# Performance work log

Hardware: AMD Instinct MI355X
Metric: run time of the kernel (lower is better)

## Reference

```python
import jax, jax.numpy as jnp
import numpy as np

N_NODES = 5000
N_EDGES = 40000
NUM_ATOM_TYPES = 100
HID = 32            # multiplicity of 0e and 1o in irreps_hidden
EDGE_ATTR_DIM = 8
NUM_BOND_TYPES = 5
OUT_SCALARS = 2 * 6 + 1  # max_charge=6 -> 13x0e
CUTOFF = 5.0
SQRT3 = 1.7320508075688772


def _sh(edge_vec):
    # o3.SphericalHarmonics('1x0e + 1x1o', normalize=True, normalization='component')
    d = jnp.sqrt(jnp.sum(edge_vec * edge_vec, axis=-1) + 1e-12)
    n = edge_vec / d[:, None]
    sh0 = jnp.ones(edge_vec.shape[0], edge_vec.dtype)          # [E]
    sh1 = SQRT3 * n[:, (1, 2, 0)]                              # [E,3], e3nn (y,z,x) order
    return sh0, sh1, d


def _soft_one_hot(d):
    # e3nn.math.soft_one_hot_linspace(d, 0, cutoff, 8, basis='gaussian', cutoff=True)
    values = jnp.linspace(0.0, CUTOFF, EDGE_ATTR_DIM + 2)[1:-1]
    step = CUTOFF / (EDGE_ATTR_DIM + 1)
    diff = (d[:, None] - values[None, :]) / step
    return jnp.exp(-diff * diff) / 1.12


def _mlp(x, W0, b0, W1, b1):
    # ScalarMLP(in, out, hidden=[in], SiLU)
    return jax.nn.silu(x @ W0 + b0) @ W1 + b1


def _tp_init(s, sh0, sh1, w):
    # FCTP(32x0e, 1x0e+1x1o -> 32x0e+32x1o); paths: 0e*0e->0e, 0e*1o->1o
    E = s.shape[0]
    w1 = w[:, : HID * HID].reshape(E, HID, HID)
    w2 = w[:, HID * HID :].reshape(E, HID, HID)
    c = 1.0 / np.sqrt(HID)  # fan-in = 32 per output irrep
    out_s = c * jnp.einsum('eu,euw->ew', s * sh0[:, None], w1)
    out_v = c * jnp.einsum('eu,ei,euw->ewi', s, sh1, w2)
    return out_s, out_v


def _tp_hidden(s, v, sh0, sh1, w):
    # FCTP(32x0e+32x1o, 1x0e+1x1o -> 32x0e+32x1o)
    # path order: 0e*0e->0e, 0e*1o->1o, 1o*0e->1o, 1o*1o->0e
    E = s.shape[0]
    ws = w.reshape(E, 4, HID, HID)
    c = 1.0 / np.sqrt(2 * HID)  # fan-in = 64 per output irrep
    dot = jnp.einsum('eui,ei->eu', v, sh1) / SQRT3  # CG(1,1->0) = delta/sqrt(3)
    out_s = c * (jnp.einsum('eu,euw->ew', s * sh0[:, None], ws[:, 0]) +
                 jnp.einsum('eu,euw->ew', dot, ws[:, 3]))
    out_v = c * (jnp.einsum('eu,ei,euw->ewi', s, sh1, ws[:, 1]) +
                 jnp.einsum('eui,euw->ewi', v * sh0[:, None, None], ws[:, 2]))
    return out_s, out_v


def _edge_tp(s1, v1, s2, v2, sh0, sh1, w):
    # FCTP(64x0e+64x1o (concat of two hidden), 1x0e+1x1o -> 5x0e)
    # blocks in concat order: s_src, v_src, s_dst, v_dst
    E = s1.shape[0]
    ws = w.reshape(E, 4, HID, NUM_BOND_TYPES)
    c = 1.0 / np.sqrt(4 * HID)  # fan-in = 128
    d1 = jnp.einsum('eui,ei->eu', v1, sh1) / SQRT3
    d2 = jnp.einsum('eui,ei->eu', v2, sh1) / SQRT3
    return c * (jnp.einsum('eu,euw->ew', s1 * sh0[:, None], ws[:, 0]) +
                jnp.einsum('eu,euw->ew', d1, ws[:, 1]) +
                jnp.einsum('eu,euw->ew', s2 * sh0[:, None], ws[:, 2]) +
                jnp.einsum('eu,euw->ew', d2, ws[:, 3]))


def _scatter_mean(ms, mv, dst, n):
    cnt = jax.ops.segment_sum(jnp.ones(dst.shape[0], ms.dtype), dst, num_segments=n)
    cnt = jnp.maximum(cnt, 1.0)
    s = jax.ops.segment_sum(ms, dst, num_segments=n) / cnt[:, None]
    v = jax.ops.segment_sum(mv, dst, num_segments=n) / cnt[:, None, None]
    return s, v


def setup_inputs() -> dict:
    key = jax.random.key(0)
    ks = jax.random.split(key, 16)
    def w(k, shape, fan_in):
        return jax.random.normal(k, shape, dtype=jnp.float32) / np.sqrt(fan_in)
    inp = {}
    inp['coordinates'] = jax.random.normal(ks[0], (N_NODES, 3), dtype=jnp.float32) * 1.5
    inp['atom_types'] = jax.random.randint(ks[1], (N_NODES,), 0, NUM_ATOM_TYPES)
    inp['edge_index'] = jax.random.randint(ks[2], (2, N_EDGES), 0, N_NODES)
    inp['atom_embed'] = jax.random.normal(ks[3], (NUM_ATOM_TYPES, HID), dtype=jnp.float32)
    inp['ip_W0'] = w(ks[4], (EDGE_ATTR_DIM, EDGE_ATTR_DIM), EDGE_ATTR_DIM)
    inp['ip_b0'] = jnp.zeros((EDGE_ATTR_DIM,), jnp.float32)
    inp['ip_W1'] = w(ks[5], (EDGE_ATTR_DIM, 2 * HID * HID), EDGE_ATTR_DIM)
    inp['ip_b1'] = jnp.zeros((2 * HID * HID,), jnp.float32)
    inp['ly_W0'] = w(ks[6], (EDGE_ATTR_DIM, EDGE_ATTR_DIM), EDGE_ATTR_DIM)
    inp['ly_b0'] = jnp.zeros((EDGE_ATTR_DIM,), jnp.float32)
    inp['ly_W1'] = w(ks[7], (EDGE_ATTR_DIM, 4 * HID * HID), EDGE_ATTR_DIM)
    inp['ly_b1'] = jnp.zeros((4 * HID * HID,), jnp.float32)
    inp['ly_Ws'] = jax.random.normal(ks[8], (HID, HID), dtype=jnp.float32)
    inp['ly_Wv'] = jax.random.normal(ks[9], (HID, HID), dtype=jnp.float32)
    inp['et_W0'] = w(ks[10], (EDGE_ATTR_DIM, EDGE_ATTR_DIM), EDGE_ATTR_DIM)
    inp['et_b0'] = jnp.zeros((EDGE_ATTR_DIM,), jnp.float32)
    inp['et_W1'] = w(ks[11], (EDGE_ATTR_DIM, 4 * HID * NUM_BOND_TYPES), EDGE_ATTR_DIM)
    inp['et_b1'] = jnp.zeros((4 * HID * NUM_BOND_TYPES,), jnp.float32)
    inp['no_W1'] = jax.random.normal(ks[12], (HID, OUT_SCALARS), dtype=jnp.float32)
    inp['no_W2'] = jax.random.normal(ks[13], (OUT_SCALARS, OUT_SCALARS), dtype=jnp.float32)
    return inp


def reference(coordinates, atom_types, edge_index, atom_embed,
              ip_W0, ip_b0, ip_W1, ip_b1,
              ly_W0, ly_b0, ly_W1, ly_b1, ly_Ws, ly_Wv,
              et_W0, et_b0, et_W1, et_b1, no_W1, no_W2):
    n = coordinates.shape[0]
    src, dst = edge_index[0], edge_index[1]
    edge_vec = coordinates[dst] - coordinates[src]
    sh0, sh1, d = _sh(edge_vec)
    edge_attr = _soft_one_hot(d)                              # [E,8]
    # initial projector: Conv(32x0e -> 32x0e+32x1o)
    s0 = atom_embed[atom_types]                               # [N,32]
    w_ip = _mlp(edge_attr, ip_W0, ip_b0, ip_W1, ip_b1)        # [E,2048]
    ms, mv = _tp_init(s0[src], sh0, sh1, w_ip)
    s, v = _scatter_mean(ms, mv, dst, n)                      # [N,32],[N,32,3]
    # one LinearSelfInteraction(Conv) layer
    w_ly = _mlp(edge_attr, ly_W0, ly_b0, ly_W1, ly_b1)        # [E,4096]
    ms, mv = _tp_hidden(s[src], v[src], sh0, sh1, w_ly)
    cs, cv = _scatter_mean(ms, mv, dst, n)
    lc = 1.0 / np.sqrt(HID)  # e3nn o3.Linear normalization
    s = cs + lc * (s @ ly_Ws)
    v = cv + lc * jnp.einsum('eui,uw->ewi', v, ly_Wv)
    # edge output: FCTP([h_src, h_dst], edge_sh) with radial weights
    w_et = _mlp(edge_attr, et_W0, et_b0, et_W1, et_b1)        # [E,640]
    edge_out = _edge_tp(s[src], v[src], s[dst], v[dst], sh0, sh1, w_et)  # [E,5]
    # node output MLP on detached scalar channel (13x0e)
    sd = jax.lax.stop_gradient(s)
    h = jax.nn.silu(sd @ no_W1 / np.sqrt(HID))
    node_out = h @ no_W2 / np.sqrt(OUT_SCALARS)               # [N,13]
    return edge_out, node_out
```

## Files before the change

### kernel.cpp

```cpp
#include <hip/hip_runtime.h>

#define NN 5000
#define NE 40000

typedef unsigned int u32;
typedef unsigned short u16;
typedef __fp16 h16x2 __attribute__((ext_vector_type(2)));
typedef _Float16 f16x8 __attribute__((ext_vector_type(8)));
typedef __attribute__((ext_vector_type(4))) float f32x4;

union AF { u32 u[4]; f16x8 v; uint4 q; };

__device__ __forceinline__ float siluf(float x) { return x / (1.f + __expf(-x)); }

__device__ __forceinline__ u32 f2bf_u(float f) {
  u32 x = __float_as_uint(f);
  return (x + 0x7FFFu + ((x >> 16) & 1u)) >> 16;
}
__device__ __forceinline__ u16 f2bf(float f) { return (u16)f2bf_u(f); }
__device__ __forceinline__ u32 packbf2(float lo, float hi) {
  return f2bf_u(lo) | (f2bf_u(hi) << 16);
}
__device__ __forceinline__ u32 pkh2(float a, float b) {
  union { h16x2 h; u32 u; } r;
  r.h = __builtin_amdgcn_cvt_pkrtz(a, b);
  return r.u;
}
__device__ __forceinline__ u16 f2h(float v) {
  _Float16 h = (_Float16)v;
  return *(u16*)&h;
}
__device__ __forceinline__ void unpack8(uint4 q, float* f) {
  f[0] = __uint_as_float(q.x << 16); f[1] = __uint_as_float(q.x & 0xFFFF0000u);
  f[2] = __uint_as_float(q.y << 16); f[3] = __uint_as_float(q.y & 0xFFFF0000u);
  f[4] = __uint_as_float(q.z << 16); f[5] = __uint_as_float(q.z & 0xFFFF0000u);
  f[6] = __uint_as_float(q.w << 16); f[7] = __uint_as_float(q.w & 0xFFFF0000u);
}
__device__ __forceinline__ float dot8f(const float* h, const float* w, float init) {
  float a = init;
#pragma unroll
  for (int k = 0; k < 8; k++) a = fmaf(h[k], w[k], a);
  return a;
}
__device__ __forceinline__ void mlp8(const float* ea, const float* __restrict__ W0,
                                     const float* __restrict__ b0, float* h) {
#pragma unroll
  for (int j = 0; j < 8; j++) {
    float a = b0[j];
#pragma unroll
    for (int i = 0; i < 8; i++) a += ea[i] * W0[i*8 + j];
    h[j] = siluf(a);
  }
}
__device__ __forceinline__ AF mkfrag(float hs, const float* s) {
  AF a;
  a.u[0] = pkh2(hs*s[0], hs*s[1]);
  a.u[1] = pkh2(hs*s[2], hs*s[3]);
  a.u[2] = pkh2(hs*s[4], hs*s[5]);
  a.u[3] = pkh2(hs*s[6], hs*s[7]);
  return a;
}

__global__ __launch_bounds__(256) void k_prep(
    const float* __restrict__ ipW1, const float* __restrict__ ipb1,
    u16* __restrict__ ipT) {
  int t0 = blockIdx.x*2304 + threadIdx.x*9;
#pragma unroll
  for (int j = 0; j < 9; j++) {
    int t = t0 + j;
    int kch = t >> 9, rem = t & 511;
    int col = rem >> 3, kk = rem & 7;
    int k = kch*8 + kk;
    int pth = col >> 5, w = col & 31;
    float v = (k < 256) ? ipW1[(k >> 5)*2048 + pth*1024 + (k & 31)*32 + w]
                        : ipb1[pth*1024 + (k - 256)*32 + w];
    ipT[t] = f2h(v);
  }
}

__global__ __launch_bounds__(256) void k_conv1(
    const float* __restrict__ coords, const int* __restrict__ eidx,
    const float* __restrict__ emb, const int* __restrict__ atype,
    const float* __restrict__ ipW0, const float* __restrict__ ipb0,
    const float* __restrict__ lyW0, const float* __restrict__ lyb0,
    const float* __restrict__ etW0, const float* __restrict__ etb0,
    const float* __restrict__ lyW1, const float* __restrict__ lyb1,
    const u16* __restrict__ ipT,
    float* __restrict__ sh, float* __restrict__ h_ly, float* __restrict__ h_et,
    int* __restrict__ cur, int* __restrict__ perm,
    u16* __restrict__ msg, u16* __restrict__ lyT) {
  if (blockIdx.x >= 625) {
    int b = blockIdx.x - 625;
    int h = b >> 3;
    int t0 = (b & 7)*2304 + threadIdx.x*9;
#pragma unroll
    for (int j = 0; j < 9; j++) {
      int t = t0 + j;
      int kch = t >> 9, rem = t & 511;
      int col = rem >> 3, kk = rem & 7;
      int k = kch*8 + kk;
      int basec = (h == 0) ? ((col >> 5)*1024 + (col & 31))
                           : ((col < 32) ? (2048 + col) : (3072 + (col - 32)));
      float v = (k < 256) ? lyW1[(k >> 5)*4096 + basec + (k & 31)*32]
                          : lyb1[basec + (k - 256)*32];
      lyT[h*18432 + t] = f2h(v);
    }
    return;
  }
  int wid = threadIdx.x >> 6, lane = threadIdx.x & 63;
  int tile = blockIdx.x*4 + wid;
  int m = lane & 15, q = lane >> 4;
  int e = tile*16 + m;
  int s = eidx[e], d = eidx[NE + e];
  int t = 0;
  if (q == 0) {
    int* cp = &cur[d];
    atomicCAS(cp, (int)0xAAAAAAAA, 0);
    t = atomicAdd(cp, 1);
    if (t < 64) perm[d*64 + t] = e;
  }
  int srow = atype[s];
  float vx = coords[d*3+0] - coords[s*3+0];
  float vy = coords[d*3+1] - coords[s*3+1];
  float vz = coords[d*3+2] - coords[s*3+2];
  float dist = sqrtf(vx*vx + vy*vy + vz*vz + 1e-12f);
  float dinv = 1.f / dist;
  const float SQ3 = 1.7320508075688772f;
  float sh0 = SQ3 * vy * dinv;
  float sh1 = SQ3 * vz * dinv;
  float sh2 = SQ3 * vx * dinv;
  float ea[8];
  const float step = 5.f / 9.f;
#pragma unroll
  for (int jj = 0; jj < 8; jj++) {
    float diff = (dist - step * (float)(jj+1)) * (9.f / 5.f);
    ea[jj] = __expf(-diff*diff) * (1.f / 1.12f);
  }
  float hip[8], hly[8], het[8];
  mlp8(ea, ipW0, ipb0, hip);
  mlp8(ea, lyW0, lyb0, hly);
  mlp8(ea, etW0, etb0, het);
  if (q == 0) {
    sh[e*3+0] = sh0; sh[e*3+1] = sh1; sh[e*3+2] = sh2;
    { float4 f0 = {hly[0],hly[1],hly[2],hly[3]}, f1 = {hly[4],hly[5],hly[6],hly[7]};
      *(float4*)&h_ly[e*8] = f0; *(float4*)&h_ly[e*8+4] = f1; }
    { float4 f0 = {het[0],het[1],het[2],het[3]}, f1 = {het[4],het[5],het[6],het[7]};
      *(float4*)&h_et[e*8] = f0; *(float4*)&h_et[e*8+4] = f1; }
  }
  float4 sA = *(const float4*)&emb[srow*32 + q*8];
  float4 sB = *(const float4*)&emb[srow*32 + q*8 + 4];
  float sf[8] = {sA.x,sA.y,sA.z,sA.w,sB.x,sB.y,sB.z,sB.w};
  f32x4 acc0 = {0.f,0.f,0.f,0.f}, acc1 = acc0, acc2 = acc0, acc3 = acc0;
  const float cs = 0.17677669529663687f;
#pragma unroll
  for (int ks = 0; ks < 9; ks++) {
    float hs = (ks < 8) ? hip[ks] : 1.f;
    AF a = mkfrag(hs, sf);
    int c2 = (ks*4 + q)*64;
    AF b0, b1f, b2, b3;
    b0.q  = *(const uint4*)&ipT[(c2 +  0 + m)*8];
    b1f.q = *(const uint4*)&ipT[(c2 + 16 + m)*8];
    b2.q  = *(const uint4*)&ipT[(c2 + 32 + m)*8];
    b3.q  = *(const uint4*)&ipT[(c2 + 48 + m)*8];
    acc0 = __builtin_amdgcn_mfma_f32_16x16x32_f16(a.v, b0.v,  acc0, 0, 0, 0);
    acc1 = __builtin_amdgcn_mfma_f32_16x16x32_f16(a.v, b1f.v, acc1, 0, 0, 0);
    acc2 = __builtin_amdgcn_mfma_f32_16x16x32_f16(a.v, b2.v,  acc2, 0, 0, 0);
    acc3 = __builtin_amdgcn_mfma_f32_16x16x32_f16(a.v, b3.v,  acc3, 0, 0, 0);
  }
#pragma unroll
  for (int r = 0; r < 4; r++) {
    int et = tile*16 + q*4 + r;
    u16* mp = msg + (size_t)et*128;
    mp[m]      = f2bf(cs*acc0[r]);
    mp[16 + m] = f2bf(cs*acc1[r]);
    float s0v = __shfl(sh0, q*4 + r, 64);
    float s1v = __shfl(sh1, q*4 + r, 64);
    float s2v = __shfl(sh2, q*4 + r, 64);
    float m0 = cs*acc2[r], m1 = cs*acc3[r];
    mp[32 +      m] = f2bf(m0*s0v);
    mp[64 +      m] = f2bf(m0*s1v);
    mp[96 +      m] = f2bf(m0*s2v);
    mp[32 + 16 + m] = f2bf(m1*s0v);
    mp[64 + 16 + m] = f2bf(m1*s1v);
    mp[96 + 16 + m] = f2bf(m1*s2v);
  }
}

__global__ __launch_bounds__(256) void k_conv2(
    const float* __restrict__ hE, const float* __restrict__ sh,
    const float* __restrict__ s1, const float* __restrict__ v1soa,
    const int* __restrict__ eidx, const u16* __restrict__ lyT,
    u16* __restrict__ msgA, u16* __restrict__ msgB) {
  int wid = threadIdx.x >> 6, lane = threadIdx.x & 63;
  const bool scalarHalf = blockIdx.x < 625;
  int blk = scalarHalf ? blockIdx.x : blockIdx.x - 625;
  int tile = blk*4 + wid;
  int m = lane & 15, q = lane >> 4;
  const u16* Bg = lyT + (scalarHalf ? 0 : 18432);
  const float c = 0.125f;
  int e = tile*16 + m;
  int srcn = eidx[e];
  float4 hA = *(const float4*)&hE[e*8];
  float4 hB = *(const float4*)&hE[e*8 + 4];
  float hf[8] = {hA.x,hA.y,hA.z,hA.w,hB.x,hB.y,hB.z,hB.w};

  if (scalarHalf) {
    float4 sA = *(const float4*)&s1[srcn*32 + q*8];
    float4 sB = *(const float4*)&s1[srcn*32 + q*8 + 4];
    float sf[8] = {sA.x,sA.y,sA.z,sA.w,sB.x,sB.y,sB.z,sB.w};
    f32x4 acc0 = {0.f,0.f,0.f,0.f}, acc1 = acc0, acc2 = acc0, acc3 = acc0;
#pragma unroll
    for (int ks = 0; ks < 9; ks++) {
      float hs = (ks < 8) ? hf[ks] : 1.f;
      AF a = mkfrag(hs, sf);
      int c2 = (ks*4 + q)*64;
      AF b0, b1f, b2, b3;
      b0.q  = *(const uint4*)&Bg[(c2 +  0 + m)*8];
      b1f.q = *(const uint4*)&Bg[(c2 + 16 + m)*8];
      b2.q  = *(const uint4*)&Bg[(c2 + 32 + m)*8];
      b3.q  = *(const uint4*)&Bg[(c2 + 48 + m)*8];
      acc0 = __builtin_amdgcn_mfma_f32_16x16x32_f16(a.v, b0.v,  acc0, 0, 0, 0);
      acc1 = __builtin_amdgcn_mfma_f32_16x16x32_f16(a.v, b1f.v, acc1, 0, 0, 0);
      acc2 = __builtin_amdgcn_mfma_f32_16x16x32_f16(a.v, b2.v,  acc2, 0, 0, 0);
      acc3 = __builtin_amdgcn_mfma_f32_16x16x32_f16(a.v, b3.v,  acc3, 0, 0, 0);
    }
#pragma unroll
    for (int r = 0; r < 4; r++) {
      int et = tile*16 + q*4 + r;
      u16* mp = msgA + (size_t)et*128;
      mp[m]      = f2bf(c*acc0[r]);
      mp[16 + m] = f2bf(c*acc1[r]);
      float s0v = sh[et*3+0], s1v = sh[et*3+1], s2v = sh[et*3+2];
      float m0 = c*acc2[r], m1 = c*acc3[r];
      mp[32 +      m] = f2bf(m0*s0v);
      mp[64 +      m] = f2bf(m0*s1v);
      mp[96 +      m] = f2bf(m0*s2v);
      mp[32 + 16 + m] = f2bf(m1*s0v);
      mp[64 + 16 + m] = f2bf(m1*s1v);
      mp[96 + 16 + m] = f2bf(m1*s2v);
    }
  } else {
    const float is3 = 0.5773502691896258f;
    float vf[3][8];
#pragma unroll
    for (int i = 0; i < 3; i++) {
      float4 aa = *(const float4*)&v1soa[i*160000 + srcn*32 + q*8];
      float4 bb = *(const float4*)&v1soa[i*160000 + srcn*32 + q*8 + 4];
      vf[i][0]=aa.x; vf[i][1]=aa.y; vf[i][2]=aa.z; vf[i][3]=aa.w;
      vf[i][4]=bb.x; vf[i][5]=bb.y; vf[i][6]=bb.z; vf[i][7]=bb.w;
    }
    float es0 = sh[e*3+0], es1 = sh[e*3+1], es2 = sh[e*3+2];
    float df[8];
#pragma unroll
    for (int j = 0; j < 8; j++)
      df[j] = (vf[0][j]*es0 + vf[1][j]*es1 + vf[2][j]*es2) * is3;
    f32x4 z = {0.f,0.f,0.f,0.f};
    f32x4 aV00 = z, aV01 = z, aV10 = z, aV11 = z, aV20 = z, aV21 = z, aD0 = z, aD1 = z;
#pragma unroll
    for (int ks = 0; ks < 9; ks++) {
      float hs = (ks < 8) ? hf[ks] : 1.f;
      int c2 = (ks*4 + q)*64;
      AF b0, b1f, b2, b3;
      b0.q  = *(const uint4*)&Bg[(c2 +  0 + m)*8];
      b1f.q = *(const uint4*)&Bg[(c2 + 16 + m)*8];
      b2.q  = *(const uint4*)&Bg[(c2 + 32 + m)*8];
      b3.q  = *(const uint4*)&Bg[(c2 + 48 + m)*8];
      AF a0 = mkfrag(hs, vf[0]);
      AF a1 = mkfrag(hs, vf[1]);
      AF a2 = mkfrag(hs, vf[2]);
      AF ad = mkfrag(hs, df);
      aV00 = __builtin_amdgcn_mfma_f32_16x16x32_f16(a0.v, b0.v,  aV00, 0, 0, 0);
      aV01 = __builtin_amdgcn_mfma_f32_16x16x32_f16(a0.v, b1f.v, aV01, 0, 0, 0);
      aV10 = __builtin_amdgcn_mfma_f32_16x16x32_f16(a1.v, b0.v,  aV10, 0, 0, 0);
      aV11 = __builtin_amdgcn_mfma_f32_16x16x32_f16(a1.v, b1f.v, aV11, 0, 0, 0);
      aV20 = __builtin_amdgcn_mfma_f32_16x16x32_f16(a2.v, b0.v,  aV20, 0, 0, 0);
      aV21 = __builtin_amdgcn_mfma_f32_16x16x32_f16(a2.v, b1f.v, aV21, 0, 0, 0);
      aD0  = __builtin_amdgcn_mfma_f32_16x16x32_f16(ad.v, b2.v,  aD0,  0, 0, 0);
      aD1  = __builtin_amdgcn_mfma_f32_16x16x32_f16(ad.v, b3.v,  aD1,  0, 0, 0);
    }
#pragma unroll
    for (int r = 0; r < 4; r++) {
      int et = tile*16 + q*4 + r;
      u16* mp = msgB + (size_t)et*128;
      mp[m]      = f2bf(c*aD0[r]);
      mp[16 + m] = f2bf(c*aD1[r]);
      mp[32 +      m] = f2bf(c*aV00[r]);
      mp[32 + 16 + m] = f2bf(c*aV01[r]);
      mp[64 +      m] = f2bf(c*aV10[r]);
      mp[64 + 16 + m] = f2bf(c*aV11[r]);
      mp[96 +      m] = f2bf(c*aV20[r]);
      mp[96 + 16 + m] = f2bf(c*aV21[r]);
    }
  }
}

__global__ __launch_bounds__(256) void k_gather1(
    const u16* __restrict__ msg, const int* __restrict__ perm,
    const int* __restrict__ cur, float* __restrict__ s1,
    float* __restrict__ v1soa) {
  __shared__ int pe[2][64];
  int ln = threadIdx.x >> 7, c = threadIdx.x & 127;
  int n = blockIdx.x*2 + ln;
  int deg = min(cur[n], 64);
  if (c < 64) pe[ln][c] = perm[n*64 + c];
  __syncthreads();
  float acc = 0.f;
  int j = 0;
  for (; j + 4 <= deg; j += 4) {
    int e0 = pe[ln][j], e1 = pe[ln][j+1], e2 = pe[ln][j+2], e3 = pe[ln][j+3];
    float x0 = __uint_as_float(((u32)msg[(size_t)e0*128 + c]) << 16);
    float x1 = __uint_as_float(((u32)msg[(size_t)e1*128 + c]) << 16);
    float x2 = __uint_as_float(((u32)msg[(size_t)e2*128 + c]) << 16);
    float x3 = __uint_as_float(((u32)msg[(size_t)e3*128 + c]) << 16);
    acc += (x0 + x1) + (x2 + x3);
  }
  for (; j < deg; j++)
    acc += __uint_as_float(((u32)msg[(size_t)pe[ln][j]*128 + c]) << 16);
  acc /= (float)max(deg, 1);
  if (c < 32) s1[n*32 + c] = acc;
  else { int i = (c-32) >> 5, w = (c-32) & 31; v1soa[i*160000 + n*32 + w] = acc; }
}

__global__ __launch_bounds__(256) void k_gather2(
    const u16* __restrict__ msgA, const u16* __restrict__ msgB,
    const int* __restrict__ perm, const int* __restrict__ cur,
    const float* __restrict__ s1, const float* __restrict__ v1soa,
    const float* __restrict__ Ws, const float* __restrict__ Wv,
    const float* __restrict__ noW1, const float* __restrict__ noW2,
    float* __restrict__ s2, float* __restrict__ v2, float* __restrict__ outN) {
  __shared__ int pe[2][64];
  __shared__ float sb[2][32];
  __shared__ float hb[2][13];
  int ln = threadIdx.x >> 7, c = threadIdx.x & 127;
  int n = blockIdx.x*2 + ln;
  int deg = min(cur[n], 64);
  if (c < 64) pe[ln][c] = perm[n*64 + c];
  __syncthreads();
  float acc = 0.f;
  int j = 0;
  for (; j + 4 <= deg; j += 4) {
    int e0 = pe[ln][j], e1 = pe[ln][j+1], e2 = pe[ln][j+2], e3 = pe[ln][j+3];
    float x0 = __uint_as_float(((u32)msgA[(size_t)e0*128 + c]) << 16)
             + __uint_as_float(((u32)msgB[(size_t)e0*128 + c]) << 16);
    float x1 = __uint_as_float(((u32)msgA[(size_t)e1*128 + c]) << 16)
             + __uint_as_float(((u32)msgB[(size_t)e1*128 + c]) << 16);
    float x2 = __uint_as_float(((u32)msgA[(size_t)e2*128 + c]) << 16)
             + __uint_as_float(((u32)msgB[(size_t)e2*128 + c]) << 16);
    float x3 = __uint_as_float(((u32)msgA[(size_t)e3*128 + c]) << 16)
             + __uint_as_float(((u32)msgB[(size_t)e3*128 + c]) << 16);
    acc += (x0 + x1) + (x2 + x3);
  }
  for (; j < deg; j++) {
    int e = pe[ln][j];
    acc += __uint_as_float(((u32)msgA[(size_t)e*128 + c]) << 16)
         + __uint_as_float(((u32)msgB[(size_t)e*128 + c]) << 16);
  }
  acc /= (float)max(deg, 1);
  const float lc = 0.17677669529663687f;
  if (c < 32) {
    float ss = 0.f;
#pragma unroll 8
    for (int u = 0; u < 32; u++) ss += s1[n*32 + u] * Ws[u*32 + c];
    float val = acc + lc*ss;
    s2[n*32 + c] = val;
    sb[ln][c] = val;
  } else {
    int i = (c-32) >> 5, w = (c-32) & 31;
    float sv = 0.f;
#pragma unroll 8
    for (int u = 0; u < 32; u++) sv += v1soa[i*160000 + n*32 + u] * Wv[u*32 + w];
    v2[n*96 + w*3 + i] = acc + lc*sv;
  }
  __syncthreads();
  const float i32 = 0.17677669529663687f;
  if (c < 13) {
    float a = 0.f;
#pragma unroll 8
    for (int u = 0; u < 32; u++) a += sb[ln][u] * noW1[u*13 + c];
    hb[ln][c] = siluf(a * i32);
  }
  __syncthreads();
  const float i13 = 0.2773500981126146f;
  if (c < 13) {
    float a = 0.f;
#pragma unroll
    for (int j2 = 0; j2 < 13; j2++) a += hb[ln][j2] * noW2[j2*13 + c];
    outN[n*13 + c] = a * i13;
  }
}

__global__ __launch_bounds__(256) void k_e3(
    const float* __restrict__ hE, const float* __restrict__ sh,
    const float* __restrict__ s2, const float* __restrict__ v2,
    const int* __restrict__ eidx,
    const float* __restrict__ W1, const float* __restrict__ b1,
    float* __restrict__ out) {
  __shared__ uint4 WQ[640];
  __shared__ float BQ[640];
  for (int t = threadIdx.x; t < 640; t += 256) {
    int u = t & 31, pw = t >> 5, p2 = pw / 5, w = pw - p2*5;
    int col = p2*160 + u*5 + w;
    const float* s = W1 + col;
    uint4 q;
    q.x = packbf2(s[0],      s[640]);
    q.y = packbf2(s[1280],   s[1920]);
    q.z = packbf2(s[2560],   s[3200]);
    q.w = packbf2(s[3840],   s[4480]);
    WQ[t] = q;
    BQ[t] = b1[col];
  }
  __syncthreads();
  const int g = threadIdx.x >> 5, tw = threadIdx.x & 31;
  const float c = 0.08838834764831845f;
  const float is3 = 0.5773502691896258f;
  for (int p = blockIdx.x*8 + g; p*2 < NE; p += gridDim.x*8) {
    int e0 = p*2, e1 = e0 + 1;
    float h0[8], h1[8];
    {
      float4 qa = *(const float4*)&hE[e0*8];
      float4 qb = *(const float4*)&hE[e0*8+4];
      h0[0]=qa.x; h0[1]=qa.y; h0[2]=qa.z; h0[3]=qa.w;
      h0[4]=qb.x; h0[5]=qb.y; h0[6]=qb.z; h0[7]=qb.w;
      float4 qc = *(const float4*)&hE[e1*8];
      float4 qd = *(const float4*)&hE[e1*8+4];
      h1[0]=qc.x; h1[1]=qc.y; h1[2]=qc.z; h1[3]=qc.w;
      h1[4]=qd.x; h1[5]=qd.y; h1[6]=qd.z; h1[7]=qd.w;
    }
    int sA = eidx[e0], dA = eidx[NE+e0];
    int sB = eidx[e1], dB = eidx[NE+e1];
    float sa0 = sh[e0*3+0], sa1 = sh[e0*3+1], sa2 = sh[e0*3+2];
    float sb0 = sh[e1*3+0], sb1 = sh[e1*3+1], sb2 = sh[e1*3+2];
    float c00 = s2[sA*32 + tw];
    float c01 = (v2[sA*96+tw*3+0]*sa0 + v2[sA*96+tw*3+1]*sa1 + v2[sA*96+tw*3+2]*sa2) * is3;
    float c02 = s2[dA*32 + tw];
    float c03 = (v2[dA*96+tw*3+0]*sa0 + v2[dA*96+tw*3+1]*sa1 + v2[dA*96+tw*3+2]*sa2) * is3;
    float c10 = s2[sB*32 + tw];
    float c11 = (v2[sB*96+tw*3+0]*sb0 + v2[sB*96+tw*3+1]*sb1 + v2[sB*96+tw*3+2]*sb2) * is3;
    float c12 = s2[dB*32 + tw];
    float c13 = (v2[dB*96+tw*3+0]*sb0 + v2[dB*96+tw*3+1]*sb1 + v2[dB*96+tw*3+2]*sb2) * is3;
    float part0[5] = {0,0,0,0,0};
    float part1[5] = {0,0,0,0,0};
#pragma unroll
    for (int pp = 0; pp < 4; pp++) {
      float cp0 = (pp==0) ? c00 : (pp==1) ? c01 : (pp==2) ? c02 : c03;
      float cp1 = (pp==0) ? c10 : (pp==1) ? c11 : (pp==2) ? c12 : c13;
#pragma unroll
      for (int w = 0; w < 5; w++) {
        int idx = (pp*5 + w)*32 + tw;
        float f[8];
        unpack8(WQ[idx], f);
        float bv = BQ[idx];
        part0[w] = fmaf(cp0, dot8f(h0, f, bv), part0[w]);
        part1[w] = fmaf(cp1, dot8f(h1, f, bv), part1[w]);
      }
    }
#pragma unroll
    for (int off = 16; off > 0; off >>= 1)
#pragma unroll
      for (int w = 0; w < 5; w++) {
        part0[w] += __shfl_xor(part0[w], off, 32);
        part1[w] += __shfl_xor(part1[w], off, 32);
      }
    float outv = 0.f;
#pragma unroll
    for (int w = 0; w < 5; w++) {
      if (tw == w)     outv = part0[w];
      if (tw == 5 + w) outv = part1[w];
    }
    if (tw < 10) out[e0*5 + tw] = c * outv;
  }
}

extern "C" void kernel_launch(void* const* d_in, const int* in_sizes, int n_in,
                              void* d_out, int out_size, void* d_ws, size_t ws_size,
                              hipStream_t stream) {
  (void)in_sizes; (void)n_in; (void)out_size; (void)ws_size;
  const float* coords = (const float*)d_in[0];
  const int*   atype  = (const int*)d_in[1];
  const int*   eidx   = (const int*)d_in[2];
  const float* emb    = (const float*)d_in[3];
  const float* ipW0 = (const float*)d_in[4];
  const float* ipb0 = (const float*)d_in[5];
  const float* ipW1 = (const float*)d_in[6];
  const float* ipb1 = (const float*)d_in[7];
  const float* lyW0 = (const float*)d_in[8];
  const float* lyb0 = (const float*)d_in[9];
  const float* lyW1 = (const float*)d_in[10];
  const float* lyb1 = (const float*)d_in[11];
  const float* lyWs = (const float*)d_in[12];
  const float* lyWv = (const float*)d_in[13];
  const float* etW0 = (const float*)d_in[14];
  const float* etb0 = (const float*)d_in[15];
  const float* etW1 = (const float*)d_in[16];
  const float* etb1 = (const float*)d_in[17];
  const float* noW1 = (const float*)d_in[18];
  const float* noW2 = (const float*)d_in[19];

  float* ws = (float*)d_ws;
  float* sh    = ws;
  float* h_ly  = ws + 440000;
  float* h_et  = ws + 760000;
  float* s1    = ws + 1240000;
  float* v1soa = ws + 1400000;
  float* s2    = ws + 1880000;
  float* v2    = ws + 2040000;
  int*   cur   = (int*)(ws + 2520000);
  int*   perm  = (int*)(ws + 2525000);
  u16*   msgA  = (u16*)(ws + 2845000);
  u16*   msgB  = (u16*)(ws + 5405000);
  u16*   lyT   = (u16*)(ws + 7965000);
  u16*   ipT   = (u16*)(ws + 7983432);

  float* outE = (float*)d_out;
  float* outN = (float*)d_out + NE*5;

  k_prep<<<8, 256, 0, stream>>>(ipW1, ipb1, ipT);
  k_conv1<<<641, 256, 0, stream>>>(coords, eidx, emb, atype,
                                   ipW0, ipb0, lyW0, lyb0, etW0, etb0,
                                   lyW1, lyb1, ipT,
                                   sh, h_ly, h_et, cur, perm, msgA, lyT);
  k_gather1<<<NN/2, 256, 0, stream>>>(msgA, perm, cur, s1, v1soa);
  k_conv2<<<1250, 256, 0, stream>>>(h_ly, sh, s1, v1soa, eidx, lyT, msgA, msgB);
  k_gather2<<<NN/2, 256, 0, stream>>>(msgA, msgB, perm, cur, s1, v1soa,
                                      lyWs, lyWv, noW1, noW2, s2, v2, outN);
  k_e3<<<1024, 256, 0, stream>>>(h_et, sh, s2, v2, eidx, etW1, etb1, outE);
}
```

Baseline: 164.5 us.

## Split conv1 and conv2 edge tiles across two wavefronts by output half

Each 16-edge tile in k_conv1 and k_conv2 is now handled by two wavefronts, each computing half of the MFMA output columns. This doubles the grid sizes to spread the work over more waves and cuts the per-wave accumulator register count, which should help occupancy and latency hiding. The cost is redundant per-edge setup in both waves, such as the edge geometry, radial basis, MLP and source feature loads. In the vector branch of k_conv2, one wave also needs all three vector components to form the dot product.

```diff
diff --git a/kernel.cpp b/kernel.cpp
--- a/kernel.cpp
+++ b/kernel.cpp
@@ -89,8 +89,8 @@
     float* __restrict__ sh, float* __restrict__ h_ly, float* __restrict__ h_et,
     int* __restrict__ cur, int* __restrict__ perm,
     u16* __restrict__ msg, u16* __restrict__ lyT) {
-  if (blockIdx.x >= 625) {
-    int b = blockIdx.x - 625;
+  if (blockIdx.x >= 1250) {
+    int b = blockIdx.x - 1250;
     int h = b >> 3;
     int t0 = (b & 7)*2304 + threadIdx.x*9;
 #pragma unroll
@@ -108,15 +108,15 @@
     return;
   }
   int wid = threadIdx.x >> 6, lane = threadIdx.x & 63;
-  int tile = blockIdx.x*4 + wid;
+  int gw = blockIdx.x*4 + wid;
+  int tile = gw >> 1, half = gw & 1;
   int m = lane & 15, q = lane >> 4;
   int e = tile*16 + m;
   int s = eidx[e], d = eidx[NE + e];
-  int t = 0;
-  if (q == 0) {
+  if (half == 0 && q == 0) {
     int* cp = &cur[d];
     atomicCAS(cp, (int)0xAAAAAAAA, 0);
-    t = atomicAdd(cp, 1);
+    int t = atomicAdd(cp, 1);
     if (t < 64) perm[d*64 + t] = e;
   }
   int srow = atype[s];
@@ -136,53 +136,72 @@
     float diff = (dist - step * (float)(jj+1)) * (9.f / 5.f);
     ea[jj] = __expf(-diff*diff) * (1.f / 1.12f);
   }
-  float hip[8], hly[8], het[8];
+  float hip[8];
   mlp8(ea, ipW0, ipb0, hip);
-  mlp8(ea, lyW0, lyb0, hly);
-  mlp8(ea, etW0, etb0, het);
-  if (q == 0) {
-    sh[e*3+0] = sh0; sh[e*3+1] = sh1; sh[e*3+2] = sh2;
-    { float4 f0 = {hly[0],hly[1],hly[2],hly[3]}, f1 = {hly[4],hly[5],hly[6],hly[7]};
-      *(float4*)&h_ly[e*8] = f0; *(float4*)&h_ly[e*8+4] = f1; }
-    { float4 f0 = {het[0],het[1],het[2],het[3]}, f1 = {het[4],het[5],het[6],het[7]};
-      *(float4*)&h_et[e*8] = f0; *(float4*)&h_et[e*8+4] = f1; }
+  if (half == 0) {
+    float hly[8], het[8];
+    mlp8(ea, lyW0, lyb0, hly);
+    mlp8(ea, etW0, etb0, het);
+    if (q == 0) {
+      sh[e*3+0] = sh0; sh[e*3+1] = sh1; sh[e*3+2] = sh2;
+      { float4 f0 = {hly[0],hly[1],hly[2],hly[3]}, f1 = {hly[4],hly[5],hly[6],hly[7]};
+        *(float4*)&h_ly[e*8] = f0; *(float4*)&h_ly[e*8+4] = f1; }
+      { float4 f0 = {het[0],het[1],het[2],het[3]}, f1 = {het[4],het[5],het[6],het[7]};
+        *(float4*)&h_et[e*8] = f0; *(float4*)&h_et[e*8+4] = f1; }
+    }
   }
   float4 sA = *(const float4*)&emb[srow*32 + q*8];
   float4 sB = *(const float4*)&emb[srow*32 + q*8 + 4];
   float sf[8] = {sA.x,sA.y,sA.z,sA.w,sB.x,sB.y,sB.z,sB.w};
-  f32x4 acc0 = {0.f,0.f,0.f,0.f}, acc1 = acc0, acc2 = acc0, acc3 = acc0;
   const float cs = 0.17677669529663687f;
-#pragma unroll
-  for (int ks = 0; ks < 9; ks++) {
-    float hs = (ks < 8) ? hip[ks] : 1.f;
-    AF a = mkfrag(hs, sf);
-    int c2 = (ks*4 + q)*64;
-    AF b0, b1f, b2, b3;
-    b0.q  = *(const uint4*)&ipT[(c2 +  0 + m)*8];
-    b1f.q = *(const uint4*)&ipT[(c2 + 16 + m)*8];
-    b2.q  = *(const uint4*)&ipT[(c2 + 32 + m)*8];
-    b3.q  = *(const uint4*)&ipT[(c2 + 48 + m)*8];
-    acc0 = __builtin_amdgcn_mfma_f32_16x16x32_f16(a.v, b0.v,  acc0, 0, 0, 0);
-    acc1 = __builtin_amdgcn_mfma_f32_16x16x32_f16(a.v, b1f.v, acc1, 0, 0, 0);
-    acc2 = __builtin_amdgcn_mfma_f32_16x16x32_f16(a.v, b2.v,  acc2, 0, 0, 0);
-    acc3 = __builtin_amdgcn_mfma_f32_16x16x32_f16(a.v, b3.v,  acc3, 0, 0, 0);
-  }
-#pragma unroll
-  for (int r = 0; r < 4; r++) {
-    int et = tile*16 + q*4 + r;
-    u16* mp = msg + (size_t)et*128;
-    mp[m]      = f2bf(cs*acc0[r]);
-    mp[16 + m] = f2bf(cs*acc1[r]);
-    float s0v = __shfl(sh0, q*4 + r, 64);
-    float s1v = __shfl(sh1, q*4 + r, 64);
-    float s2v = __shfl(sh2, q*4 + r, 64);
-    float m0 = cs*acc2[r], m1 = cs*acc3[r];
-    mp[32 +      m] = f2bf(m0*s0v);
-    mp[64 +      m] = f2bf(m0*s1v);
-    mp[96 +      m] = f2bf(m0*s2v);
-    mp[32 + 16 + m] = f2bf(m1*s0v);
-    mp[64 + 16 + m] = f2bf(m1*s1v);
-    mp[96 + 16 + m] = f2bf(m1*s2v);
+  if (half == 0) {
+    f32x4 acc0 = {0.f,0.f,0.f,0.f}, acc1 = acc0;
+#pragma unroll
+    for (int ks = 0; ks < 9; ks++) {
+      float hs = (ks < 8) ? hip[ks] : 1.f;
+      AF a = mkfrag(hs, sf);
+      int c2 = (ks*4 + q)*64;
+      AF b0, b1f;
+      b0.q  = *(const uint4*)&ipT[(c2 +  0 + m)*8];
+      b1f.q = *(const uint4*)&ipT[(c2 + 16 + m)*8];
+      acc0 = __builtin_amdgcn_mfma_f32_16x16x32_f16(a.v, b0.v,  acc0, 0, 0, 0);
+      acc1 = __builtin_amdgcn_mfma_f32_16x16x32_f16(a.v, b1f.v, acc1, 0, 0, 0);
+    }
+#pragma unroll
+    for (int r = 0; r < 4; r++) {
+      int et = tile*16 + q*4 + r;
+      u16* mp = msg + (size_t)et*128;
+      mp[m]      = f2bf(cs*acc0[r]);
+      mp[16 + m] = f2bf(cs*acc1[r]);
+    }
+  } else {
+    f32x4 acc2 = {0.f,0.f,0.f,0.f}, acc3 = acc2;
+#pragma unroll
+    for (int ks = 0; ks < 9; ks++) {
+      float hs = (ks < 8) ? hip[ks] : 1.f;
+      AF a = mkfrag(hs, sf);
+      int c2 = (ks*4 + q)*64;
+      AF b2, b3;
+      b2.q = *(const uint4*)&ipT[(c2 + 32 + m)*8];
+      b3.q = *(const uint4*)&ipT[(c2 + 48 + m)*8];
+      acc2 = __builtin_amdgcn_mfma_f32_16x16x32_f16(a.v, b2.v, acc2, 0, 0, 0);
+      acc3 = __builtin_amdgcn_mfma_f32_16x16x32_f16(a.v, b3.v, acc3, 0, 0, 0);
+    }
+#pragma unroll
+    for (int r = 0; r < 4; r++) {
+      int et = tile*16 + q*4 + r;
+      u16* mp = msg + (size_t)et*128;
+      float s0v = __shfl(sh0, q*4 + r, 64);
+      float s1v = __shfl(sh1, q*4 + r, 64);
+      float s2v = __shfl(sh2, q*4 + r, 64);
+      float m0 = cs*acc2[r], m1 = cs*acc3[r];
+      mp[32 +      m] = f2bf(m0*s0v);
+      mp[64 +      m] = f2bf(m0*s1v);
+      mp[96 +      m] = f2bf(m0*s2v);
+      mp[32 + 16 + m] = f2bf(m1*s0v);
+      mp[64 + 16 + m] = f2bf(m1*s1v);
+      mp[96 + 16 + m] = f2bf(m1*s2v);
+    }
   }
 }
 
@@ -192,11 +211,12 @@
     const int* __restrict__ eidx, const u16* __restrict__ lyT,
     u16* __restrict__ msgA, u16* __restrict__ msgB) {
   int wid = threadIdx.x >> 6, lane = threadIdx.x & 63;
-  const bool scalarHalf = blockIdx.x < 625;
-  int blk = scalarHalf ? blockIdx.x : blockIdx.x - 625;
-  int tile = blk*4 + wid;
+  int gw = blockIdx.x*4 + wid;
+  const bool scalarKind = gw < 5000;
+  int t2 = scalarKind ? gw : gw - 5000;
+  int tile = t2 >> 1, half = t2 & 1;
   int m = lane & 15, q = lane >> 4;
-  const u16* Bg = lyT + (scalarHalf ? 0 : 18432);
+  const u16* Bg = lyT + (scalarKind ? 0 : 18432);
   const float c = 0.125f;
   int e = tile*16 + m;
   int srcn = eidx[e];
@@ -204,92 +224,135 @@
   float4 hB = *(const float4*)&hE[e*8 + 4];
   float hf[8] = {hA.x,hA.y,hA.z,hA.w,hB.x,hB.y,hB.z,hB.w};
 
-  if (scalarHalf) {
+  if (scalarKind) {
     float4 sA = *(const float4*)&s1[srcn*32 + q*8];
     float4 sB = *(const float4*)&s1[srcn*32 + q*8 + 4];
     float sf[8] = {sA.x,sA.y,sA.z,sA.w,sB.x,sB.y,sB.z,sB.w};
-    f32x4 acc0 = {0.f,0.f,0.f,0.f}, acc1 = acc0, acc2 = acc0, acc3 = acc0;
-#pragma unroll
-    for (int ks = 0; ks < 9; ks++) {
-      float hs = (ks < 8) ? hf[ks] : 1.f;
-      AF a = mkfrag(hs, sf);
-      int c2 = (ks*4 + q)*64;
-      AF b0, b1f, b2, b3;
-      b0.q  = *(const uint4*)&Bg[(c2 +  0 + m)*8];
-      b1f.q = *(const uint4*)&Bg[(c2 + 16 + m)*8];
-      b2.q  = *(const uint4*)&Bg[(c2 + 32 + m)*8];
-      b3.q  = *(const uint4*)&Bg[(c2 + 48 + m)*8];
-      acc0 = __builtin_amdgcn_mfma_f32_16x16x32_f16(a.v, b0.v,  acc0, 0, 0, 0);
-      acc1 = __builtin_amdgcn_mfma_f32_16x16x32_f16(a.v, b1f.v, acc1, 0, 0, 0);
-      acc2 = __builtin_amdgcn_mfma_f32_16x16x32_f16(a.v, b2.v,  acc2, 0, 0, 0);
-      acc3 = __builtin_amdgcn_mfma_f32_16x16x32_f16(a.v, b3.v,  acc3, 0, 0, 0);
-    }
-#pragma unroll
-    for (int r = 0; r < 4; r++) {
-      int et = tile*16 + q*4 + r;
-      u16* mp = msgA + (size_t)et*128;
-      mp[m]      = f2bf(c*acc0[r]);
-      mp[16 + m] = f2bf(c*acc1[r]);
-      float s0v = sh[et*3+0], s1v = sh[et*3+1], s2v = sh[et*3+2];
-      float m0 = c*acc2[r], m1 = c*acc3[r];
-      mp[32 +      m] = f2bf(m0*s0v);
-      mp[64 +      m] = f2bf(m0*s1v);
-      mp[96 +      m] = f2bf(m0*s2v);
-      mp[32 + 16 + m] = f2bf(m1*s0v);
-      mp[64 + 16 + m] = f2bf(m1*s1v);
-      mp[96 + 16 + m] = f2bf(m1*s2v);
+    if (half == 0) {
+      f32x4 acc0 = {0.f,0.f,0.f,0.f}, acc1 = acc0;
+#pragma unroll
+      for (int ks = 0; ks < 9; ks++) {
+        float hs = (ks < 8) ? hf[ks] : 1.f;
+        AF a = mkfrag(hs, sf);
+        int c2 = (ks*4 + q)*64;
+        AF b0, b1f;
+        b0.q  = *(const uint4*)&Bg[(c2 +  0 + m)*8];
+        b1f.q = *(const uint4*)&Bg[(c2 + 16 + m)*8];
+        acc0 = __builtin_amdgcn_mfma_f32_16x16x32_f16(a.v, b0.v,  acc0, 0, 0, 0);
+        acc1 = __builtin_amdgcn_mfma_f32_16x16x32_f16(a.v, b1f.v, acc1, 0, 0, 0);
+      }
+#pragma unroll
+      for (int r = 0; r < 4; r++) {
+        int et = tile*16 + q*4 + r;
+        u16* mp = msgA + (size_t)et*128;
+        mp[m]      = f2bf(c*acc0[r]);
+        mp[16 + m] = f2bf(c*acc1[r]);
+      }
+    } else {
+      f32x4 acc2 = {0.f,0.f,0.f,0.f}, acc3 = acc2;
+#pragma unroll
+      for (int ks = 0; ks < 9; ks++) {
+        float hs = (ks < 8) ? hf[ks] : 1.f;
+        AF a = mkfrag(hs, sf);
+        int c2 = (ks*4 + q)*64;
+        AF b2, b3;
+        b2.q = *(const uint4*)&Bg[(c2 + 32 + m)*8];
+        b3.q = *(const uint4*)&Bg[(c2 + 48 + m)*8];
+        acc2 = __builtin_amdgcn_mfma_f32_16x16x32_f16(a.v, b2.v, acc2, 0, 0, 0);
+        acc3 = __builtin_amdgcn_mfma_f32_16x16x32_f16(a.v, b3.v, acc3, 0, 0, 0);
+      }
+#pragma unroll
+      for (int r = 0; r < 4; r++) {
+        int et = tile*16 + q*4 + r;
+        u16* mp = msgA + (size_t)et*128;
+        float s0v = sh[et*3+0], s1v = sh[et*3+1], s2v = sh[et*3+2];
+        float m0 = c*acc2[r], m1 = c*acc3[r];
+        mp[32 +      m] = f2bf(m0*s0v);
+        mp[64 +      m] = f2bf(m0*s1v);
+        mp[96 +      m] = f2bf(m0*s2v);
+        mp[32 + 16 + m] = f2bf(m1*s0v);
+        mp[64 + 16 + m] = f2bf(m1*s1v);
+        mp[96 + 16 + m] = f2bf(m1*s2v);
+      }
     }
   } else {
     const float is3 = 0.5773502691896258f;
-    float vf[3][8];
-#pragma unroll
-    for (int i = 0; i < 3; i++) {
-      float4 aa = *(const float4*)&v1soa[i*160000 + srcn*32 + q*8];
-      float4 bb = *(const float4*)&v1soa[i*160000 + srcn*32 + q*8 + 4];
-      vf[i][0]=aa.x; vf[i][1]=aa.y; vf[i][2]=aa.z; vf[i][3]=aa.w;
-      vf[i][4]=bb.x; vf[i][5]=bb.y; vf[i][6]=bb.z; vf[i][7]=bb.w;
-    }
-    float es0 = sh[e*3+0], es1 = sh[e*3+1], es2 = sh[e*3+2];
-    float df[8];
-#pragma unroll
-    for (int j = 0; j < 8; j++)
-      df[j] = (vf[0][j]*es0 + vf[1][j]*es1 + vf[2][j]*es2) * is3;
-    f32x4 z = {0.f,0.f,0.f,0.f};
-    f32x4 aV00 = z, aV01 = z, aV10 = z, aV11 = z, aV20 = z, aV21 = z, aD0 = z, aD1 = z;
-#pragma unroll
-    for (int ks = 0; ks < 9; ks++) {
-      float hs = (ks < 8) ? hf[ks] : 1.f;
-      int c2 = (ks*4 + q)*64;
-      AF b0, b1f, b2, b3;
-      b0.q  = *(const uint4*)&Bg[(c2 +  0 + m)*8];
-      b1f.q = *(const uint4*)&Bg[(c2 + 16 + m)*8];
-      b2.q  = *(const uint4*)&Bg[(c2 + 32 + m)*8];
-      b3.q  = *(const uint4*)&Bg[(c2 + 48 + m)*8];
-      AF a0 = mkfrag(hs, vf[0]);
-      AF a1 = mkfrag(hs, vf[1]);
-      AF a2 = mkfrag(hs, vf[2]);
-      AF ad = mkfrag(hs, df);
-      aV00 = __builtin_amdgcn_mfma_f32_16x16x32_f16(a0.v, b0.v,  aV00, 0, 0, 0);
-      aV01 = __builtin_amdgcn_mfma_f32_16x16x32_f16(a0.v, b1f.v, aV01, 0, 0, 0);
-      aV10 = __builtin_amdgcn_mfma_f32_16x16x32_f16(a1.v, b0.v,  aV10, 0, 0, 0);
-      aV11 = __builtin_amdgcn_mfma_f32_16x16x32_f16(a1.v, b1f.v, aV11, 0, 0, 0);
-      aV20 = __builtin_amdgcn_mfma_f32_16x16x32_f16(a2.v, b0.v,  aV20, 0, 0, 0);
-      aV21 = __builtin_amdgcn_mfma_f32_16x16x32_f16(a2.v, b1f.v, aV21, 0, 0, 0);
-      aD0  = __builtin_amdgcn_mfma_f32_16x16x32_f16(ad.v, b2.v,  aD0,  0, 0, 0);
-      aD1  = __builtin_amdgcn_mfma_f32_16x16x32_f16(ad.v, b3.v,  aD1,  0, 0, 0);
-    }
-#pragma unroll
-    for (int r = 0; r < 4; r++) {
-      int et = tile*16 + q*4 + r;
-      u16* mp = msgB + (size_t)et*128;
-      mp[m]      = f2bf(c*aD0[r]);
-      mp[16 + m] = f2bf(c*aD1[r]);
-      mp[32 +      m] = f2bf(c*aV00[r]);
-      mp[32 + 16 + m] = f2bf(c*aV01[r]);
-      mp[64 +      m] = f2bf(c*aV10[r]);
-      mp[64 + 16 + m] = f2bf(c*aV11[r]);
-      mp[96 +      m] = f2bf(c*aV20[r]);
-      mp[96 + 16 + m] = f2bf(c*aV21[r]);
+    if (half == 0) {
+      float vf0[8], vf1[8];
+#pragma unroll
+      for (int i = 0; i < 2; i++) {
+        float* dst = (i == 0) ? vf0 : vf1;
+        float4 aa = *(const float4*)&v1soa[i*160000 + srcn*32 + q*8];
+        float4 bb = *(const float4*)&v1soa[i*160000 + srcn*32 + q*8 + 4];
+        dst[0]=aa.x; dst[1]=aa.y; dst[2]=aa.z; dst[3]=aa.w;
+        dst[4]=bb.x; dst[5]=bb.y; dst[6]=bb.z; dst[7]=bb.w;
+      }
+      f32x4 z = {0.f,0.f,0.f,0.f};
+      f32x4 aV00 = z, aV01 = z, aV10 = z, aV11 = z;
+#pragma unroll
+      for (int ks = 0; ks < 9; ks++) {
+        float hs = (ks < 8) ? hf[ks] : 1.f;
+        int c2 = (ks*4 + q)*64;
+        AF b0, b1f;
+        b0.q  = *(const uint4*)&Bg[(c2 +  0 + m)*8];
+        b1f.q = *(const uint4*)&Bg[(c2 + 16 + m)*8];
+        AF a0 = mkfrag(hs, vf0);
+        AF a1 = mkfrag(hs, vf1);
+        aV00 = __builtin_amdgcn_mfma_f32_16x16x32_f16(a0.v, b0.v,  aV00, 0, 0, 0);
+        aV01 = __builtin_amdgcn_mfma_f32_16x16x32_f16(a0.v, b1f.v, aV01, 0, 0, 0);
+        aV10 = __builtin_amdgcn_mfma_f32_16x16x32_f16(a1.v, b0.v,  aV10, 0, 0, 0);
+        aV11 = __builtin_amdgcn_mfma_f32_16x16x32_f16(a1.v, b1f.v, aV11, 0, 0, 0);
+      }
+#pragma unroll
+      for (int r = 0; r < 4; r++) {
+        int et = tile*16 + q*4 + r;
+        u16* mp = msgB + (size_t)et*128;
+        mp[32 +      m] = f2bf(c*aV00[r]);
+        mp[32 + 16 + m] = f2bf(c*aV01[r]);
+        mp[64 +      m] = f2bf(c*aV10[r]);
+        mp[64 + 16 + m] = f2bf(c*aV11[r]);
+      }
+    } else {
+      float vf[3][8];
+#pragma unroll
+      for (int i = 0; i < 3; i++) {
+        float4 aa = *(const float4*)&v1soa[i*160000 + srcn*32 + q*8];
+        float4 bb = *(const float4*)&v1soa[i*160000 + srcn*32 + q*8 + 4];
+        vf[i][0]=aa.x; vf[i][1]=aa.y; vf[i][2]=aa.z; vf[i][3]=aa.w;
+        vf[i][4]=bb.x; vf[i][5]=bb.y; vf[i][6]=bb.z; vf[i][7]=bb.w;
+      }
+      float es0 = sh[e*3+0], es1 = sh[e*3+1], es2 = sh[e*3+2];
+      float df[8];
+#pragma unroll
+      for (int j = 0; j < 8; j++)
+        df[j] = (vf[0][j]*es0 + vf[1][j]*es1 + vf[2][j]*es2) * is3;
+      f32x4 z = {0.f,0.f,0.f,0.f};
+      f32x4 aV20 = z, aV21 = z, aD0 = z, aD1 = z;
+#pragma unroll
+      for (int ks = 0; ks < 9; ks++) {
+        float hs = (ks < 8) ? hf[ks] : 1.f;
+        int c2 = (ks*4 + q)*64;
+        AF b0, b1f, b2, b3;
+        b0.q  = *(const uint4*)&Bg[(c2 +  0 + m)*8];
+        b1f.q = *(const uint4*)&Bg[(c2 + 16 + m)*8];
+        b2.q  = *(const uint4*)&Bg[(c2 + 32 + m)*8];
+        b3.q  = *(const uint4*)&Bg[(c2 + 48 + m)*8];
+        AF a2 = mkfrag(hs, vf[2]);
+        AF ad = mkfrag(hs, df);
+        aV20 = __builtin_amdgcn_mfma_f32_16x16x32_f16(a2.v, b0.v,  aV20, 0, 0, 0);
+        aV21 = __builtin_amdgcn_mfma_f32_16x16x32_f16(a2.v, b1f.v, aV21, 0, 0, 0);
+        aD0  = __builtin_amdgcn_mfma_f32_16x16x32_f16(ad.v, b2.v,  aD0,  0, 0, 0);
+        aD1  = __builtin_amdgcn_mfma_f32_16x16x32_f16(ad.v, b3.v,  aD1,  0, 0, 0);
+      }
+#pragma unroll
+      for (int r = 0; r < 4; r++) {
+        int et = tile*16 + q*4 + r;
+        u16* mp = msgB + (size_t)et*128;
+        mp[m]       = f2bf(c*aD0[r]);
+        mp[16 + m]  = f2bf(c*aD1[r]);
+        mp[96 +      m] = f2bf(c*aV20[r]);
+        mp[96 + 16 + m] = f2bf(c*aV21[r]);
+      }
     }
   }
 }
@@ -515,12 +578,12 @@
   float* outN = (float*)d_out + NE*5;
 
   k_prep<<<8, 256, 0, stream>>>(ipW1, ipb1, ipT);
-  k_conv1<<<641, 256, 0, stream>>>(coords, eidx, emb, atype,
-                                   ipW0, ipb0, lyW0, lyb0, etW0, etb0,
-                                   lyW1, lyb1, ipT,
-                                   sh, h_ly, h_et, cur, perm, msgA, lyT);
+  k_conv1<<<1266, 256, 0, stream>>>(coords, eidx, emb, atype,
+                                    ipW0, ipb0, lyW0, lyb0, etW0, etb0,
+                                    lyW1, lyb1, ipT,
+                                    sh, h_ly, h_et, cur, perm, msgA, lyT);
   k_gather1<<<NN/2, 256, 0, stream>>>(msgA, perm, cur, s1, v1soa);
-  k_conv2<<<1250, 256, 0, stream>>>(h_ly, sh, s1, v1soa, eidx, lyT, msgA, msgB);
+  k_conv2<<<2500, 256, 0, stream>>>(h_ly, sh, s1, v1soa, eidx, lyT, msgA, msgB);
   k_gather2<<<NN/2, 256, 0, stream>>>(msgA, msgB, perm, cur, s1, v1soa,
                                       lyWs, lyWv, noW1, noW2, s2, v2, outN);
   k_e3<<<1024, 256, 0, stream>>>(h_et, sh, s2, v2, eidx, etW1, etb1, outE);
```

Result: no change. 166.3 us (+1.1%).
